# Optimization experiments

Hardware: AMD Instinct MI355X
Metric: run time of the kernel (lower is better)

## Reference

```python
import jax, jax.numpy as jnp
import numpy as np

EMB_DIM = 512
N_HEAD = 8
EPS = 1e-5


def gen_pos_emb(emb_dim, max_len):
    half = emb_dim // 2
    r = 10000.0 ** (-1.0 / half)
    freq = r ** jnp.arange(half, dtype=jnp.float32)  # cumprod of [1, r, r, ...]
    phase = jnp.arange(max_len, dtype=jnp.float32)[:, None] * freq[None, :]  # [L, half]
    pe = jnp.zeros((max_len, emb_dim), dtype=jnp.float32)
    pe = pe.at[:, 0::2].set(jnp.sin(phase)).at[:, 1::2].set(jnp.cos(phase))
    return pe  # [L, E]


def setup_inputs() -> dict:
    key = jax.random.key(0)
    ks = jax.random.split(key, 12)
    bs, L, E, H, V = 8, 2048, EMB_DIM, N_HEAD, 32000
    inputs = jax.random.randint(ks[0], (bs, L), 0, V, dtype=jnp.int64 if jax.config.jax_enable_x64 else jnp.int32)
    lens = jnp.sort(jax.random.randint(ks[1], (bs,), 1, L + 1, dtype=jnp.int32))
    lens = lens.at[-1].set(L)  # model requires lens[-1] == max_len
    s = 0.02
    emb_table = (jax.random.normal(ks[2], (V, E), jnp.float32) * s).at[0].set(0.0)  # padding_idx=0
    qkv_w = jax.random.normal(ks[3], (3 * E, E), jnp.float32) * s
    qkv_b = jax.random.normal(ks[4], (3 * E,), jnp.float32) * s
    gn_w = jnp.ones((H,), jnp.float32)
    gn_b = jnp.zeros((H,), jnp.float32)
    ln_w = jnp.ones((E,), jnp.float32)
    ln_b = jnp.zeros((E,), jnp.float32)
    w1 = jax.random.normal(ks[5], (2 * E, E), jnp.float32) * s
    b1 = jax.random.normal(ks[6], (2 * E,), jnp.float32) * s
    w2 = jax.random.normal(ks[7], (E, 2 * E), jnp.float32) * s
    b2 = jax.random.normal(ks[8], (E,), jnp.float32) * s
    return {"inputs": inputs, "lens": lens, "emb_table": emb_table, "qkv_w": qkv_w,
            "qkv_b": qkv_b, "gn_w": gn_w, "gn_b": gn_b, "ln_w": ln_w, "ln_b": ln_b,
            "w1": w1, "b1": b1, "w2": w2, "b2": b2}


def _forward(inputs, lens, emb_table, qkv_w, qkv_b, gn_w, gn_b, ln_w, ln_b, w1, b1, w2, b2):
    bs, L = inputs.shape
    E, H = EMB_DIM, N_HEAD
    dh = E // H
    scaling = (E / H) ** -0.5

    # embedding + positional encoding; torch works seq-major: emb [L, bs, E]
    emb = emb_table[inputs.T] + gen_pos_emb(E, L)[:, None, :]

    # qkv projection and head split
    qkv = emb @ qkv_w.T + qkv_b                      # [L, bs, 3E]
    qkv = qkv.reshape(L, bs * H, 3 * dh).transpose(1, 0, 2)  # [B=bs*H, L, 3dh]
    q, k, v = jnp.split(qkv, 3, axis=-1)             # each [B, L, dh]

    # attention-sum: softmax over keys with zero-score mask, then sum over queries
    scores = jnp.einsum('bqd,bkd->bqk', q, k) * scaling   # [B, L, L]
    mask = scores == 0
    aw = jax.nn.softmax(jnp.where(mask, -jnp.inf, scores), axis=-1)
    aw = jnp.where(mask, 0.0, aw).sum(axis=-2)            # [B, L]

    attn_out = jnp.einsum('bl,bld->bd', aw, v).reshape(bs, H, dh)  # [bs, H, dh]

    # GroupNorm(n_head, n_head): per-channel normalization over dh with affine
    mu = attn_out.mean(-1, keepdims=True)
    var = attn_out.var(-1, keepdims=True)
    attn_out = (attn_out - mu) * jax.lax.rsqrt(var + EPS)
    attn_out = attn_out * gn_w[None, :, None] + gn_b[None, :, None]
    ft = attn_out.reshape(bs, E)

    # post_process: residual with length-normalized sum of embeddings
    x = ft + emb.sum(0) / lens.astype(emb.dtype)[:, None]  # [bs, E]

    # LayerNorm -> Linear -> tanh -> Linear, residual
    m = x.mean(-1, keepdims=True)
    vv = x.var(-1, keepdims=True)
    xn = (x - m) * jax.lax.rsqrt(vv + EPS) * ln_w + ln_b
    ff = jnp.tanh(xn @ w1.T + b1) @ w2.T + b2
    return x + ff


def reference(inputs, lens, emb_table, qkv_w, qkv_b, gn_w, gn_b, ln_w, ln_b, w1, b1, w2, b2):
    return _forward(inputs, lens, emb_table, qkv_w, qkv_b, gn_w, gn_b, ln_w, ln_b, w1, b1, w2, b2)
```

## Files before the change

### kernel.cpp

```cpp
#include <hip/hip_runtime.h>
#include <math.h>

#define L_SEQ 2048
#define BS 8
#define EMB 512
#define NHEAD 8
#define DH 64
#define NB (BS*NHEAD)
#define SCALE_Q 0.18033688f

typedef short short8  __attribute__((ext_vector_type(8)));
typedef short short4v __attribute__((ext_vector_type(4)));
typedef float f32x4   __attribute__((ext_vector_type(4)));

__device__ __forceinline__ short f2bf(float x) {
    unsigned u = __float_as_uint(x);
    unsigned r = (u + 0x7FFFu + ((u >> 16) & 1u)) >> 16;
    return (short)r;
}
__device__ __forceinline__ float bf2f(short h) {
    return __uint_as_float(((unsigned)(unsigned short)h) << 16);
}

__global__ void freq_kernel(float* __restrict__ freq) {
    int j = threadIdx.x;
    double r = pow(10000.0, -1.0 / 256.0);
    float rf = (float)r;
    freq[j] = (float)pow((double)rf, (double)j);
}

__global__ __launch_bounds__(256) void pe_kernel(const float* __restrict__ freq,
                                                 float* __restrict__ pe) {
    int l = blockIdx.x;
    int j = threadIdx.x;
    float ph = (float)l * freq[j];
    pe[l*EMB + 2*j]     = sinf(ph);
    pe[l*EMB + 2*j + 1] = cosf(ph);
}

__global__ __launch_bounds__(256) void embed_kernel(const int* __restrict__ inputs,
                                                    const float* __restrict__ table,
                                                    const float* __restrict__ pe,
                                                    float* __restrict__ emb,
                                                    short* __restrict__ ahi,
                                                    short* __restrict__ alo) {
    int idx = blockIdx.x*256 + threadIdx.x;
    int e4 = idx & 127;
    int rb = idx >> 7;
    int b  = rb & 7;
    int l  = rb >> 3;
    int tok = inputs[b*L_SEQ + l];
    float4 tv = reinterpret_cast<const float4*>(table)[(size_t)tok*128 + e4];
    float4 pv = reinterpret_cast<const float4*>(pe)[(size_t)l*128 + e4];
    float4 o;
    o.x = tv.x + pv.x; o.y = tv.y + pv.y; o.z = tv.z + pv.z; o.w = tv.w + pv.w;
    reinterpret_cast<float4*>(emb)[(size_t)rb*128 + e4] = o;
    int e0   = e4 * 4;
    int tile = rb >> 4;
    int ks   = e0 >> 5;
    int lane = (rb & 15) + (((e0 >> 3) & 3) << 4);
    int j0   = e0 & 7;
    size_t off = ((((size_t)tile*16 + ks) << 6) + lane)*8 + j0;
    float v[4] = {o.x, o.y, o.z, o.w};
    short4v h4, l4;
    #pragma unroll
    for (int q = 0; q < 4; q++) {
        short hb = f2bf(v[q]);
        h4[q] = hb;
        l4[q] = f2bf(v[q] - bf2f(hb));
    }
    *reinterpret_cast<short4v*>(ahi + off) = h4;
    *reinterpret_cast<short4v*>(alo + off) = l4;
}

__global__ __launch_bounds__(256) void embsum_kernel(const float* __restrict__ emb,
                                                     float* __restrict__ embsum) {
    int b  = blockIdx.x;
    int ec = blockIdx.y;
    int lc = blockIdx.z;
    int e  = ec*256 + threadIdx.x;
    float s = 0.f;
    int l0 = lc*128;
    for (int l = l0; l < l0+128; l++)
        s += emb[((size_t)l*BS + b)*EMB + e];
    atomicAdd(&embsum[b*EMB + e], s);
}

__global__ __launch_bounds__(256) void wsplit_kernel(const float* __restrict__ src,
                                                     short8* __restrict__ hi,
                                                     short8* __restrict__ lo) {
    int idx = blockIdx.x*256 + threadIdx.x;
    int c = idx & 63;
    int r = idx >> 6;
    const float4* s4 = reinterpret_cast<const float4*>(src + (size_t)r*512 + c*8);
    float4 f0 = s4[0], f1 = s4[1];
    int ks   = c >> 2;
    int lane = (r & 15) + ((c & 3) << 4);
    int tile = r >> 4;
    float v[8] = {f0.x,f0.y,f0.z,f0.w,f1.x,f1.y,f1.z,f1.w};
    short8 h8, l8;
    #pragma unroll
    for (int q = 0; q < 8; q++) {
        short hb = f2bf(v[q]);
        h8[q] = hb;
        l8[q] = f2bf(v[q] - bf2f(hb));
    }
    size_t o = (((size_t)tile*16 + ks) << 6) + lane;
    hi[o] = h8; lo[o] = l8;
}

__global__ __launch_bounds__(256) void qkv_mfma_kernel(const short8* __restrict__ ahi,
                                                       const short8* __restrict__ alo,
                                                       const short8* __restrict__ bhi,
                                                       const short8* __restrict__ blo,
                                                       const float* __restrict__ bias,
                                                       short* __restrict__ qh,
                                                       short* __restrict__ kh,
                                                       float* __restrict__ vg) {
    __shared__ short8 sA[2][8][64];
    __shared__ short8 sB[2][8][64];
    int id  = blockIdx.x;
    int xcd = id & 7, pos = id >> 3;
    int nb  = pos % 12;
    int mb  = xcd*16 + pos/12;
    int t  = threadIdx.x;
    int w  = t >> 6, lane = t & 63;
    int wr = w >> 1, wc = w & 1;

    f32x4 acc[4][4];
    #pragma unroll
    for (int i = 0; i < 4; i++)
        #pragma unroll
        for (int j = 0; j < 4; j++)
            acc[i][j] = (f32x4){0.f, 0.f, 0.f, 0.f};

    short8 stg[8];
    #pragma unroll
    for (int i = 0; i < 8; i++) {
        int li = w*8 + i;
        int h = li & 1, ti = (li >> 1) & 7, isB = li >> 4;
        const short8* base = isB ? (h ? blo : bhi) : (h ? alo : ahi);
        int gt = isB ? (nb*8 + ti) : (mb*8 + ti);
        stg[i] = base[(((size_t)gt*16 + 0) << 6) + lane];
    }
    for (int ks = 0; ks < 16; ks++) {
        __syncthreads();
        #pragma unroll
        for (int i = 0; i < 8; i++) {
            int li = w*8 + i;
            int h = li & 1, ti = (li >> 1) & 7, isB = li >> 4;
            if (isB) sB[h][ti][lane] = stg[i];
            else     sA[h][ti][lane] = stg[i];
        }
        __syncthreads();
        if (ks < 15) {
            #pragma unroll
            for (int i = 0; i < 8; i++) {
                int li = w*8 + i;
                int h = li & 1, ti = (li >> 1) & 7, isB = li >> 4;
                const short8* base = isB ? (h ? blo : bhi) : (h ? alo : ahi);
                int gt = isB ? (nb*8 + ti) : (mb*8 + ti);
                stg[i] = base[(((size_t)gt*16 + (ks+1)) << 6) + lane];
            }
        }
        short8 Ah[4], Al[4];
        #pragma unroll
        for (int fi = 0; fi < 4; fi++) {
            Ah[fi] = sA[0][wr*4 + fi][lane];
            Al[fi] = sA[1][wr*4 + fi][lane];
        }
        #pragma unroll
        for (int fj = 0; fj < 4; fj++) {
            short8 Bh = sB[0][wc*4 + fj][lane];
            short8 Bl = sB[1][wc*4 + fj][lane];
            #pragma unroll
            for (int fi = 0; fi < 4; fi++) {
                acc[fi][fj] = __builtin_amdgcn_mfma_f32_16x16x32_bf16(Ah[fi], Bh, acc[fi][fj], 0, 0, 0);
                acc[fi][fj] = __builtin_amdgcn_mfma_f32_16x16x32_bf16(Ah[fi], Bl, acc[fi][fj], 0, 0, 0);
                acc[fi][fj] = __builtin_amdgcn_mfma_f32_16x16x32_bf16(Al[fi], Bh, acc[fi][fj], 0, 0, 0);
            }
        }
    }
    int row0 = (lane >> 4) * 4;
    int col  = lane & 15;
    #pragma unroll
    for (int fj = 0; fj < 4; fj++) {
        int n   = nb*128 + wc*64 + fj*16 + col;
        int h   = n / 192;
        int sel = (n % 192) / 64;
        float bn = bias[n];
        int nn = n & 63;
        #pragma unroll
        for (int fi = 0; fi < 4; fi++) {
            int m0 = mb*128 + wr*64 + fi*16 + row0;
            #pragma unroll
            for (int r = 0; r < 4; r++) {
                int m = m0 + r;
                int l = m >> 3, b = m & 7;
                size_t o = (((size_t)(b*NHEAD + h))*L_SEQ + l)*DH + nn;
                float val = acc[fi][fj][r] + bn;
                if (sel == 2)      vg[o] = val;
                else if (sel == 1) kh[o] = f2bf(val);
                else               qh[o] = f2bf(val * SCALE_Q);
            }
        }
    }
}

__global__ __launch_bounds__(256) void reformat16_kernel(const short* __restrict__ src,
                                                         short8* __restrict__ dst) {
    int idx = blockIdx.x*256 + threadIdx.x;
    int c  = idx & 7;
    int r  = (idx >> 3) & 2047;
    int bh = idx >> 14;
    short8 v = *reinterpret_cast<const short8*>(src + ((size_t)bh*L_SEQ + r)*DH + c*8);
    int ks   = c >> 2;
    int lane = (r & 15) + ((c & 3) << 4);
    int tile = r >> 4;
    dst[(((size_t)(bh*128 + tile)*2 + ks) << 6) + lane] = v;
}

__global__ __launch_bounds__(256) void ml_mfma_kernel(const short8* __restrict__ qbf,
                                                      const short8* __restrict__ kbf,
                                                      float* __restrict__ cq) {
    int bh = blockIdx.x, wv = threadIdx.x >> 6, lane = threadIdx.x & 63;
    int z  = blockIdx.z;
    int qt0 = (blockIdx.y*4 + wv)*4;
    short8 bq0[4], bq1[4];
    #pragma unroll
    for (int j = 0; j < 4; j++) {
        const short8* qp = qbf + (((size_t)(bh*128 + qt0 + j)*2) << 6) + lane;
        bq0[j] = qp[0]; bq1[j] = qp[64];
    }
    const short8* kp = kbf + ((size_t)bh << 14) + lane + (size_t)z*64*128;
    float lsum[4] = {0.f, 0.f, 0.f, 0.f};
    for (int t = 0; t < 64; t++) {
        short8 a0 = kp[0], a1 = kp[64];
        kp += 128;
        #pragma unroll
        for (int j = 0; j < 4; j++) {
            f32x4 acc = {0.f, 0.f, 0.f, 0.f};
            acc = __builtin_amdgcn_mfma_f32_16x16x32_bf16(a0, bq0[j], acc, 0, 0, 0);
            acc = __builtin_amdgcn_mfma_f32_16x16x32_bf16(a1, bq1[j], acc, 0, 0, 0);
            #pragma unroll
            for (int r = 0; r < 4; r++)
                lsum[j] += (acc[r] != 0.f) ? __builtin_amdgcn_exp2f(acc[r]) : 0.f;
        }
    }
    #pragma unroll
    for (int j = 0; j < 4; j++) {
        lsum[j] += __shfl_xor(lsum[j], 16);
        lsum[j] += __shfl_xor(lsum[j], 32);
    }
    if (lane < 16) {
        #pragma unroll
        for (int j = 0; j < 4; j++)
            atomicAdd(&cq[(size_t)bh*L_SEQ + (qt0+j)*16 + lane], lsum[j]);
    }
}

__global__ __launch_bounds__(256) void kw_mfma_kernel(const short8* __restrict__ qbf,
                                                      const short8* __restrict__ kbf,
                                                      const float* __restrict__ cq,
                                                      float* __restrict__ wk) {
    int bh = blockIdx.x, wv = threadIdx.x >> 6, lane = threadIdx.x & 63;
    int z  = blockIdx.z;
    int kt0 = (blockIdx.y*4 + wv)*4;
    short8 bk0[4], bk1[4];
    #pragma unroll
    for (int j = 0; j < 4; j++) {
        const short8* kp = kbf + (((size_t)(bh*128 + kt0 + j)*2) << 6) + lane;
        bk0[j] = kp[0]; bk1[j] = kp[64];
    }
    const short8* qp = qbf + ((size_t)bh << 14) + lane + (size_t)z*64*128;
    const float4* cp = reinterpret_cast<const float4*>(cq + (size_t)bh*L_SEQ) + (lane >> 4) + z*64*4;
    float w[4] = {0.f, 0.f, 0.f, 0.f};
    for (int t = 0; t < 64; t++) {
        short8 a0 = qp[0], a1 = qp[64];
        qp += 128;
        float4 c4 = cp[0]; cp += 4;
        float cr[4];
        cr[0] = (c4.x > 0.f) ? __builtin_amdgcn_rcpf(c4.x) : 0.f;
        cr[1] = (c4.y > 0.f) ? __builtin_amdgcn_rcpf(c4.y) : 0.f;
        cr[2] = (c4.z > 0.f) ? __builtin_amdgcn_rcpf(c4.z) : 0.f;
        cr[3] = (c4.w > 0.f) ? __builtin_amdgcn_rcpf(c4.w) : 0.f;
        #pragma unroll
        for (int j = 0; j < 4; j++) {
            f32x4 acc = {0.f, 0.f, 0.f, 0.f};
            acc = __builtin_amdgcn_mfma_f32_16x16x32_bf16(a0, bk0[j], acc, 0, 0, 0);
            acc = __builtin_amdgcn_mfma_f32_16x16x32_bf16(a1, bk1[j], acc, 0, 0, 0);
            #pragma unroll
            for (int r = 0; r < 4; r++) {
                float p = __builtin_amdgcn_exp2f(acc[r]);
                w[j] += (acc[r] != 0.f) ? p*cr[r] : 0.f;
            }
        }
    }
    #pragma unroll
    for (int j = 0; j < 4; j++) {
        w[j] += __shfl_xor(w[j], 16);
        w[j] += __shfl_xor(w[j], 32);
    }
    if (lane < 16) {
        #pragma unroll
        for (int j = 0; j < 4; j++)
            atomicAdd(&wk[(size_t)bh*L_SEQ + (kt0+j)*16 + lane], w[j]);
    }
}

__global__ __launch_bounds__(256) void pv_kernel(const float* __restrict__ vg,
                                                 const float* __restrict__ wk,
                                                 float* __restrict__ O) {
    __shared__ float red[256];
    int bidx = blockIdx.x;
    int seg  = blockIdx.y;
    int t    = threadIdx.x;
    int d    = t & 63;
    int ks   = t >> 6;
    const float* vrow = vg + ((size_t)bidx*L_SEQ + seg*256)*DH;
    const float* wrow = wk + (size_t)bidx*L_SEQ + seg*256;
    float acc = 0.f;
    for (int k = ks; k < 256; k += 4)
        acc += wrow[k] * vrow[k*64 + d];
    red[t] = acc;
    __syncthreads();
    if (t < 128) red[t] += red[t + 128];
    __syncthreads();
    if (t < 64) atomicAdd(&O[bidx*64 + t], red[t] + red[t + 64]);
}

__global__ __launch_bounds__(256) void ln_kernel(const float* __restrict__ O,
                                                 const float* __restrict__ embsum,
                                                 const int* __restrict__ lens,
                                                 const float* __restrict__ gn_w,
                                                 const float* __restrict__ gn_b,
                                                 const float* __restrict__ ln_w,
                                                 const float* __restrict__ ln_b,
                                                 float* __restrict__ xbuf,
                                                 float* __restrict__ xnbuf) {
    int b = blockIdx.x;
    int t = threadIdx.x;
    __shared__ float x[EMB];
    __shared__ float rbuf[16];
    {
        int h = t >> 5;
        int i32 = t & 31;
        float v0 = O[b*EMB + h*64 + i32];
        float v1 = O[b*EMB + h*64 + i32 + 32];
        float s = v0+v1, ss = v0*v0 + v1*v1;
        #pragma unroll
        for (int off = 16; off >= 1; off >>= 1) {
            s  += __shfl_xor(s,  off, 32);
            ss += __shfl_xor(ss, off, 32);
        }
        float mu  = s * (1.f/64.f);
        float var = ss * (1.f/64.f) - mu*mu;
        float rstd = rsqrtf(var + 1e-5f);
        float gw = gn_w[h], gb = gn_b[h];
        float len = (float)lens[b];
        x[h*64+i32]    = (v0-mu)*rstd*gw + gb + embsum[b*EMB + h*64+i32] / len;
        x[h*64+i32+32] = (v1-mu)*rstd*gw + gb + embsum[b*EMB + h*64+i32+32] / len;
    }
    __syncthreads();
    float xv0 = x[t], xv1 = x[t+256];
    {
        float s = xv0+xv1, ss = xv0*xv0 + xv1*xv1;
        #pragma unroll
        for (int off = 32; off >= 1; off >>= 1) {
            s  += __shfl_xor(s,  off);
            ss += __shfl_xor(ss, off);
        }
        int wid = t >> 6;
        if ((t & 63) == 0) { rbuf[wid] = s; rbuf[8+wid] = ss; }
        __syncthreads();
        float S  = rbuf[0]+rbuf[1]+rbuf[2]+rbuf[3];
        float SS = rbuf[8]+rbuf[9]+rbuf[10]+rbuf[11];
        float mu  = S * (1.f/512.f);
        float var = SS * (1.f/512.f) - mu*mu;
        float rstd = rsqrtf(var + 1e-5f);
        xnbuf[b*EMB + t]       = (xv0-mu)*rstd*ln_w[t]     + ln_b[t];
        xnbuf[b*EMB + t + 256] = (xv1-mu)*rstd*ln_w[t+256] + ln_b[t+256];
        xbuf[b*EMB + t]        = xv0;
        xbuf[b*EMB + t + 256]  = xv1;
    }
}

__global__ __launch_bounds__(256) void mlp1_kernel(const float* __restrict__ xnbuf,
                                                   const float* __restrict__ w1,
                                                   const float* __restrict__ b1,
                                                   float* __restrict__ h1buf) {
    __shared__ float sxn[BS][EMB];
    int t = threadIdx.x;
    #pragma unroll
    for (int i = 0; i < 4; i++)
        reinterpret_cast<float4*>(&sxn[0][0])[t + 256*i] =
            reinterpret_cast<const float4*>(xnbuf)[t + 256*i];
    __syncthreads();
    int b = t & 7;
    int j = blockIdx.x*32 + (t >> 3);
    const float4* wr = reinterpret_cast<const float4*>(w1 + (size_t)j*512);
    const float4* xr = reinterpret_cast<const float4*>(&sxn[b][0]);
    float a0 = 0.f, a1 = 0.f;
    #pragma unroll 8
    for (int i = 0; i < 128; i += 2) {
        float4 wv = wr[i],   xv = xr[i];
        a0 += wv.x*xv.x + wv.y*xv.y + wv.z*xv.z + wv.w*xv.w;
        float4 wv1 = wr[i+1], xv1 = xr[i+1];
        a1 += wv1.x*xv1.x + wv1.y*xv1.y + wv1.z*xv1.z + wv1.w*xv1.w;
    }
    h1buf[b*1024 + j] = tanhf(a0 + a1 + b1[j]);
}

__global__ __launch_bounds__(256) void mlp2_kernel(const float* __restrict__ h1buf,
                                                   const float* __restrict__ xbuf,
                                                   const float* __restrict__ w2,
                                                   const float* __restrict__ b2,
                                                   float* __restrict__ out) {
    __shared__ float sh1[BS][2*EMB];
    int t = threadIdx.x;
    #pragma unroll
    for (int i = 0; i < 8; i++)
        reinterpret_cast<float4*>(&sh1[0][0])[t + 256*i] =
            reinterpret_cast<const float4*>(h1buf)[t + 256*i];
    __syncthreads();
    int b = t & 7;
    int e = blockIdx.x*32 + (t >> 3);
    const float4* wr = reinterpret_cast<const float4*>(w2 + (size_t)e*1024);
    const float4* hr = reinterpret_cast<const float4*>(&sh1[b][0]);
    float a0 = 0.f, a1 = 0.f;
    #pragma unroll 8
    for (int i = 0; i < 256; i += 2) {
        float4 wv = wr[i],   hv = hr[i];
        a0 += wv.x*hv.x + wv.y*hv.y + wv.z*hv.z + wv.w*hv.w;
        float4 wv1 = wr[i+1], hv1 = hr[i+1];
        a1 += wv1.x*hv1.x + wv1.y*hv1.y + wv1.z*hv1.z + wv1.w*hv1.w;
    }
    out[b*EMB + e] = xbuf[b*EMB + e] + a0 + a1 + b2[e];
}

extern "C" void kernel_launch(void* const* d_in, const int* in_sizes, int n_in,
                              void* d_out, int out_size, void* d_ws, size_t ws_size,
                              hipStream_t stream) {
    const int*   inputs    = (const int*)d_in[0];
    const int*   lens      = (const int*)d_in[1];
    const float* emb_table = (const float*)d_in[2];
    const float* qkv_w     = (const float*)d_in[3];
    const float* qkv_b     = (const float*)d_in[4];
    const float* gn_w      = (const float*)d_in[5];
    const float* gn_b      = (const float*)d_in[6];
    const float* ln_w      = (const float*)d_in[7];
    const float* ln_b      = (const float*)d_in[8];
    const float* w1        = (const float*)d_in[9];
    const float* b1        = (const float*)d_in[10];
    const float* w2        = (const float*)d_in[11];
    const float* b2        = (const float*)d_in[12];
    float* out = (float*)d_out;

    float* ws = (float*)d_ws;
    const size_t NE = (size_t)L_SEQ*BS*EMB;
    float* emb    = ws;
    float* vg     = emb + NE;
    float* pe     = vg  + NE;
    float* afrag  = pe  + (size_t)L_SEQ*EMB;
    short* ahi_s  = reinterpret_cast<short*>(afrag);
    short* alo_s  = ahi_s + NE;
    float* qkrows = afrag + NE;
    short* qh     = reinterpret_cast<short*>(qkrows);
    short* kh     = qh + NE;
    float* wfrag  = qkrows + NE;
    short8* bhi   = reinterpret_cast<short8*>(wfrag);
    short8* blo   = bhi + 98304;
    float* cqbuf  = wfrag + 786432;
    float* wkbuf  = cqbuf + (size_t)NB*L_SEQ;
    float* freq   = wkbuf + (size_t)NB*L_SEQ;
    float* embsum = freq + 256;
    float* Oacc   = embsum + BS*EMB;
    float* xbuf   = Oacc + NB*DH;
    float* xnbuf  = xbuf + BS*EMB;
    float* h1buf  = xnbuf + BS*EMB;
    short8* kbf = reinterpret_cast<short8*>(emb);
    short8* qbf = kbf + (size_t)NB*128*2*64;

    hipMemsetAsync(embsum, 0, 2*BS*EMB*sizeof(float), stream);
    hipMemsetAsync(cqbuf, 0, 2*(size_t)NB*L_SEQ*sizeof(float), stream);

    freq_kernel<<<1, 256, 0, stream>>>(freq);
    pe_kernel<<<L_SEQ, 256, 0, stream>>>(freq, pe);
    embed_kernel<<<(L_SEQ*BS*(EMB/4))/256, 256, 0, stream>>>(inputs, emb_table, pe, emb,
                                                             ahi_s, alo_s);
    embsum_kernel<<<dim3(BS, 2, 16), 256, 0, stream>>>(emb, embsum);
    wsplit_kernel<<<384, 256, 0, stream>>>(qkv_w, bhi, blo);
    qkv_mfma_kernel<<<1536, 256, 0, stream>>>(reinterpret_cast<const short8*>(ahi_s),
                                              reinterpret_cast<const short8*>(alo_s),
                                              bhi, blo, qkv_b, qh, kh, vg);
    reformat16_kernel<<<4096, 256, 0, stream>>>(kh, kbf);
    reformat16_kernel<<<4096, 256, 0, stream>>>(qh, qbf);
    ml_mfma_kernel<<<dim3(NB, 8, 2), 256, 0, stream>>>(qbf, kbf, cqbuf);
    kw_mfma_kernel<<<dim3(NB, 8, 2), 256, 0, stream>>>(qbf, kbf, cqbuf, wkbuf);
    pv_kernel<<<dim3(NB, 8), 256, 0, stream>>>(vg, wkbuf, Oacc);
    ln_kernel<<<BS, 256, 0, stream>>>(Oacc, embsum, lens, gn_w, gn_b, ln_w, ln_b, xbuf, xnbuf);
    mlp1_kernel<<<32, 256, 0, stream>>>(xnbuf, w1, b1, h1buf);
    mlp2_kernel<<<16, 256, 0, stream>>>(h1buf, xbuf, w2, b2, out);
}
```

Baseline: 422.4 us.

## Write Q/K in MFMA fragment layout from QKV epilogue and split key range further

The QKV projection epilogue now stores the bf16 Q and K values directly in the tiled MFMA fragment layout. This removes both reformat16 kernel launches and the intermediate row-major Q/K buffers, along with their extra global round-trip. The ml and kw attention kernels now split the sequence dimension into 4 chunks instead of 2, doubling the grid to raise parallelism, with more atomic accumulation in exchange. The two memsets are merged into one contiguous clear. The fused epilogue's scattered 2-byte stores may coalesce less well than the old row-major writes.

```diff
diff --git a/kernel.cpp b/kernel.cpp
--- a/kernel.cpp
+++ b/kernel.cpp
@@ -114,8 +114,8 @@
                                                        const short8* __restrict__ bhi,
                                                        const short8* __restrict__ blo,
                                                        const float* __restrict__ bias,
-                                                       short* __restrict__ qh,
-                                                       short* __restrict__ kh,
+                                                       short* __restrict__ qbf_s,
+                                                       short* __restrict__ kbf_s,
                                                        float* __restrict__ vg) {
     __shared__ short8 sA[2][8][64];
     __shared__ short8 sB[2][8][64];
@@ -197,27 +197,21 @@
             for (int r = 0; r < 4; r++) {
                 int m = m0 + r;
                 int l = m >> 3, b = m & 7;
-                size_t o = (((size_t)(b*NHEAD + h))*L_SEQ + l)*DH + nn;
                 float val = acc[fi][fj][r] + bn;
-                if (sel == 2)      vg[o] = val;
-                else if (sel == 1) kh[o] = f2bf(val);
-                else               qh[o] = f2bf(val * SCALE_Q);
+                if (sel == 2) {
+                    vg[(((size_t)(b*NHEAD + h))*L_SEQ + l)*DH + nn] = val;
+                } else {
+                    int bh   = b*NHEAD + h;
+                    int tile = l >> 4;
+                    int kss  = nn >> 5;
+                    int ln2  = (l & 15) + (((nn >> 3) & 3) << 4);
+                    size_t off = ((((size_t)(bh*128 + tile)*2 + kss) << 6) + ln2)*8 + (nn & 7);
+                    if (sel == 1) kbf_s[off] = f2bf(val);
+                    else          qbf_s[off] = f2bf(val * SCALE_Q);
+                }
             }
         }
     }
-}
-
-__global__ __launch_bounds__(256) void reformat16_kernel(const short* __restrict__ src,
-                                                         short8* __restrict__ dst) {
-    int idx = blockIdx.x*256 + threadIdx.x;
-    int c  = idx & 7;
-    int r  = (idx >> 3) & 2047;
-    int bh = idx >> 14;
-    short8 v = *reinterpret_cast<const short8*>(src + ((size_t)bh*L_SEQ + r)*DH + c*8);
-    int ks   = c >> 2;
-    int lane = (r & 15) + ((c & 3) << 4);
-    int tile = r >> 4;
-    dst[(((size_t)(bh*128 + tile)*2 + ks) << 6) + lane] = v;
 }
 
 __global__ __launch_bounds__(256) void ml_mfma_kernel(const short8* __restrict__ qbf,
@@ -232,9 +226,9 @@
         const short8* qp = qbf + (((size_t)(bh*128 + qt0 + j)*2) << 6) + lane;
         bq0[j] = qp[0]; bq1[j] = qp[64];
     }
-    const short8* kp = kbf + ((size_t)bh << 14) + lane + (size_t)z*64*128;
+    const short8* kp = kbf + ((size_t)bh << 14) + lane + (size_t)z*4096;
     float lsum[4] = {0.f, 0.f, 0.f, 0.f};
-    for (int t = 0; t < 64; t++) {
+    for (int t = 0; t < 32; t++) {
         short8 a0 = kp[0], a1 = kp[64];
         kp += 128;
         #pragma unroll
@@ -272,10 +266,10 @@
         const short8* kp = kbf + (((size_t)(bh*128 + kt0 + j)*2) << 6) + lane;
         bk0[j] = kp[0]; bk1[j] = kp[64];
     }
-    const short8* qp = qbf + ((size_t)bh << 14) + lane + (size_t)z*64*128;
-    const float4* cp = reinterpret_cast<const float4*>(cq + (size_t)bh*L_SEQ) + (lane >> 4) + z*64*4;
+    const short8* qp = qbf + ((size_t)bh << 14) + lane + (size_t)z*4096;
+    const float4* cp = reinterpret_cast<const float4*>(cq + (size_t)bh*L_SEQ) + (lane >> 4) + z*128;
     float w[4] = {0.f, 0.f, 0.f, 0.f};
-    for (int t = 0; t < 64; t++) {
+    for (int t = 0; t < 32; t++) {
         short8 a0 = qp[0], a1 = qp[64];
         qp += 128;
         float4 c4 = cp[0]; cp += 4;
@@ -465,8 +459,6 @@
     short* ahi_s  = reinterpret_cast<short*>(afrag);
     short* alo_s  = ahi_s + NE;
     float* qkrows = afrag + NE;
-    short* qh     = reinterpret_cast<short*>(qkrows);
-    short* kh     = qh + NE;
     float* wfrag  = qkrows + NE;
     short8* bhi   = reinterpret_cast<short8*>(wfrag);
     short8* blo   = bhi + 98304;
@@ -481,8 +473,7 @@
     short8* kbf = reinterpret_cast<short8*>(emb);
     short8* qbf = kbf + (size_t)NB*128*2*64;
 
-    hipMemsetAsync(embsum, 0, 2*BS*EMB*sizeof(float), stream);
-    hipMemsetAsync(cqbuf, 0, 2*(size_t)NB*L_SEQ*sizeof(float), stream);
+    hipMemsetAsync(cqbuf, 0, (2*(size_t)NB*L_SEQ + 256 + 2*BS*EMB) * sizeof(float), stream);
 
     freq_kernel<<<1, 256, 0, stream>>>(freq);
     pe_kernel<<<L_SEQ, 256, 0, stream>>>(freq, pe);
@@ -492,11 +483,11 @@
     wsplit_kernel<<<384, 256, 0, stream>>>(qkv_w, bhi, blo);
     qkv_mfma_kernel<<<1536, 256, 0, stream>>>(reinterpret_cast<const short8*>(ahi_s),
                                               reinterpret_cast<const short8*>(alo_s),
-                                              bhi, blo, qkv_b, qh, kh, vg);
-    reformat16_kernel<<<4096, 256, 0, stream>>>(kh, kbf);
-    reformat16_kernel<<<4096, 256, 0, stream>>>(qh, qbf);
-    ml_mfma_kernel<<<dim3(NB, 8, 2), 256, 0, stream>>>(qbf, kbf, cqbuf);
-    kw_mfma_kernel<<<dim3(NB, 8, 2), 256, 0, stream>>>(qbf, kbf, cqbuf, wkbuf);
+                                              bhi, blo, qkv_b,
+                                              reinterpret_cast<short*>(qbf),
+                                              reinterpret_cast<short*>(kbf), vg);
+    ml_mfma_kernel<<<dim3(NB, 8, 4), 256, 0, stream>>>(qbf, kbf, cqbuf);
+    kw_mfma_kernel<<<dim3(NB, 8, 4), 256, 0, stream>>>(qbf, kbf, cqbuf, wkbuf);
     pv_kernel<<<dim3(NB, 8), 256, 0, stream>>>(vg, wkbuf, Oacc);
     ln_kernel<<<BS, 256, 0, stream>>>(Oacc, embsum, lens, gn_w, gn_b, ln_w, ln_b, xbuf, xnbuf);
     mlp1_kernel<<<32, 256, 0, stream>>>(xnbuf, w1, b1, h1buf);
```

Result: faster. 400.9 us (-5.1%).
